# Kernel optimization log

Hardware: AMD Instinct MI355X
Metric: run time of the kernel (lower is better)

Reference implementation:

```python
import jax, jax.numpy as jnp
import numpy as np


def setup_inputs() -> dict:
    key = jax.random.key(0)
    kq, kk, kv, km = jax.random.split(key, 4)
    B, H, S, D = 2, 16, 2048, 64
    q = jax.random.normal(kq, (B, H, S, D), dtype=jnp.float32)
    k = jax.random.normal(kk, (B, H, S, D), dtype=jnp.float32)
    v = jax.random.normal(kv, (B, H, S, D), dtype=jnp.float32)
    mask = jax.random.randint(km, (B, 1, S, D * S // D), 0, 2).astype(bool)
    return {"q": q, "k": k, "v": v, "mask": mask, "d_k": 64}


def reference(q, k, v, mask, d_k):
    # score = q @ k^T / sqrt(d_k), masked_fill(mask, -1e9)
    scale = jnp.float32(1.0 / np.sqrt(d_k))
    score = jnp.einsum("bhsd,bhtd->bhst", q, k) * scale  # [B,H,S,S]
    score = jnp.where(mask, jnp.float32(-1e9), score)
    attention = jax.nn.softmax(score, axis=-1)
    # NOTE: original module (faithfully) multiplies the RAW masked score by v,
    # not the softmaxed attention: results = score @ v
    results = jnp.einsum("bhst,bhtd->bhsd", score, v)
    return (results, attention)
```

## Files before the change

kernel.cpp:

```cpp
#include <hip/hip_runtime.h>

typedef __attribute__((ext_vector_type(8))) short short8;
typedef __attribute__((ext_vector_type(4))) float f32x4;

#define S_LEN 2048
#define DH 64

__device__ __forceinline__ unsigned short f2bf(float x) {
  unsigned u = __builtin_bit_cast(unsigned, x);
  u += 0x7fffu + ((u >> 16) & 1u);
  return (unsigned short)(u >> 16);
}

__global__ void detect_stride_k(const unsigned char* __restrict__ m, int* flag) {
  __shared__ int any;
  if (threadIdx.x == 0) any = 0;
  __syncthreads();
  int acc = 0;
  for (int i = threadIdx.x; i < 4096; i += 256)
    if (i & 3) acc |= m[i];
  if (acc) atomicOr(&any, 1);
  __syncthreads();
  if (threadIdx.x == 0) *flag = any ? 1 : 4;
}

__global__ void prep_kernel(const float* __restrict__ k,
                            const float* __restrict__ v,
                            const unsigned char* __restrict__ m,
                            const int* __restrict__ flagp,
                            char* __restrict__ kbf,
                            char* __restrict__ vtbf,
                            unsigned* __restrict__ bits) {
  int bid = blockIdx.x;
  if (bid < 2048) {
    int idx = bid * 256 + threadIdx.x;
    const float4* s = (const float4*)k + (size_t)idx * 2;
    float4 a = s[0], b = s[1];
    int4 o;
    o.x = (int)f2bf(a.x) | ((int)f2bf(a.y) << 16);
    o.y = (int)f2bf(a.z) | ((int)f2bf(a.w) << 16);
    o.z = (int)f2bf(b.x) | ((int)f2bf(b.y) << 16);
    o.w = (int)f2bf(b.z) | ((int)f2bf(b.w) << 16);
    ((int4*)kbf)[idx] = o;
  } else if (bid < 6144) {
    int gt = (bid - 2048) * 256 + threadIdx.x;
    int wid = gt >> 6;
    int lane = gt & 63;
    int bh = wid >> 9;
    int rem = wid & 511;
    int d0 = (rem >> 5) * 4;
    int t = (rem & 31) * 64 + lane;
    float4 val = *(const float4*)(v + ((size_t)bh * S_LEN + t) * DH + d0);
    unsigned short* o = (unsigned short*)vtbf;
    size_t base = ((size_t)bh * DH + d0) * S_LEN + t;
    o[base]             = f2bf(val.x);
    o[base + S_LEN]     = f2bf(val.y);
    o[base + 2 * S_LEN] = f2bf(val.z);
    o[base + 3 * S_LEN] = f2bf(val.w);
  } else {
    int idx = (bid - 6144) * 256 + threadIdx.x;
    unsigned wword = 0;
    if (*flagp == 1) {
      const uint4* p = (const uint4*)(m + (size_t)idx * 32);
      uint4 a = p[0], bq = p[1];
      unsigned arr[8] = {a.x, a.y, a.z, a.w, bq.x, bq.y, bq.z, bq.w};
#pragma unroll
      for (int d = 0; d < 8; ++d)
#pragma unroll
        for (int j = 0; j < 4; ++j)
          wword |= (((arr[d] >> (8 * j)) & 255u) != 0u ? 1u : 0u) << (d * 4 + j);
    } else {
      const uint4* p = (const uint4*)m + (size_t)idx * 8;
#pragma unroll
      for (int d = 0; d < 8; ++d) {
        uint4 vv = p[d];
        wword |= (vv.x ? 1u : 0u) << (d * 4);
        wword |= (vv.y ? 1u : 0u) << (d * 4 + 1);
        wword |= (vv.z ? 1u : 0u) << (d * 4 + 2);
        wword |= (vv.w ? 1u : 0u) << (d * 4 + 3);
      }
    }
    bits[idx] = wword;
  }
}

__global__ __launch_bounds__(512, 4)
void attn_fused(const float* __restrict__ qsrc,
                const unsigned* __restrict__ mbits,
                const char* __restrict__ kbf,
                const char* __restrict__ vtbf,
                float* __restrict__ out) {
  __shared__ __align__(16) char smem[81920];

  const int tid = threadIdx.x;
  const int lane = tid & 63;
  const int w = tid >> 6;
  const int l15 = lane & 15;
  const int g = lane >> 4;
  const int sw = (l15 & 7) << 4;

  int raw = blockIdx.x;
  int swz = (raw & 7) * 64 + (raw >> 3);
  const int bh = swz >> 4;
  const int qblk = swz & 15;
  const int b = bh >> 4;
  const int q0 = qblk * 128 + w * 16;

  const char* ksrc_bh = kbf + (size_t)bh * (S_LEN * DH * 2);
  const char* vsrc_bh = vtbf + (size_t)bh * (DH * S_LEN * 2);
  char* pb = smem + 65536 + w * 2048;

  const unsigned* mrow = mbits + (size_t)b * (S_LEN * (S_LEN / 32)) +
                         (size_t)(q0 + l15) * (S_LEN / 32);

  auto stageK = [&](int buf, int t0) {
    char* dst = smem + buf * 16384;
#pragma unroll
    for (int it = 0; it < 2; ++it) {
      int o = (w * 2 + it) * 1024 + lane * 16;
      int r = o >> 7;
      int inner = o & 127;
      const char* gp = ksrc_bh + (size_t)t0 * 128 + r * 128 + (inner ^ ((r & 7) << 4));
      __builtin_amdgcn_global_load_lds((const unsigned*)gp,
                                       (unsigned*)(dst + (w * 2 + it) * 1024), 16, 0, 0);
    }
  };
  auto stageV = [&](int buf, int t0) {
    char* dst = smem + 32768 + buf * 16384;
#pragma unroll
    for (int it = 0; it < 2; ++it) {
      int o = (w * 2 + it) * 1024 + lane * 16;
      int r = o >> 8;
      int inner = o & 255;
      const char* gp = vsrc_bh + (size_t)t0 * 2 + (size_t)r * (S_LEN * 2) +
                       (inner ^ ((r & 7) << 4));
      __builtin_amdgcn_global_load_lds((const unsigned*)gp,
                                       (unsigned*)(dst + (w * 2 + it) * 1024), 16, 0, 0);
    }
  };

  short8 qf[2];
#pragma unroll
  for (int kc = 0; kc < 2; ++kc) {
    const float* qp = qsrc + ((size_t)bh * S_LEN + q0 + l15) * DH + 32 * kc + 8 * g;
    float4 x = *(const float4*)qp;
    float4 y = *(const float4*)(qp + 4);
    short8 f;
    f[0] = (short)f2bf(x.x); f[1] = (short)f2bf(x.y);
    f[2] = (short)f2bf(x.z); f[3] = (short)f2bf(x.w);
    f[4] = (short)f2bf(y.x); f[5] = (short)f2bf(y.y);
    f[6] = (short)f2bf(y.z); f[7] = (short)f2bf(y.w);
    qf[kc] = f;
  }

  f32x4 acc[4];
#pragma unroll
  for (int i = 0; i < 4; ++i) acc[i] = (f32x4){0.f, 0.f, 0.f, 0.f};
  float lp = 0.f;

  stageK(0, 0);
  stageV(0, 0);
  uint4 mw = *(const uint4*)mrow;
  __syncthreads();
  int cur = 0;

  for (int t0 = 0; t0 < S_LEN; t0 += 128) {
    uint4 mw_n;
    if (t0 + 128 < S_LEN) {
      stageK(cur ^ 1, t0 + 128);
      stageV(cur ^ 1, t0 + 128);
      mw_n = *(const uint4*)(mrow + (t0 + 128) / 32);
    }
    const char* kbuf = smem + cur * 16384;
    const char* vbuf = smem + 32768 + cur * 16384;

    f32x4 sf[8];
#pragma unroll
    for (int tc = 0; tc < 8; ++tc) {
      const char* rowp = kbuf + (16 * tc + l15) * 128;
      short8 a0 = *(const short8*)(rowp + ((16 * g) ^ sw));
      short8 a1 = *(const short8*)(rowp + ((64 + 16 * g) ^ sw));
      f32x4 z = (f32x4){0.f, 0.f, 0.f, 0.f};
      f32x4 t00 = __builtin_amdgcn_mfma_f32_16x16x32_bf16(a0, qf[0], z, 0, 0, 0);
      sf[tc] = __builtin_amdgcn_mfma_f32_16x16x32_bf16(a1, qf[1], t00, 0, 0, 0);
    }

    const unsigned mwa[4] = {mw.x, mw.y, mw.z, mw.w};
#pragma unroll
    for (int h = 0; h < 2; ++h) {
      char* pbr = pb + l15 * 128;
#pragma unroll
      for (int tq = 0; tq < 4; ++tq) {
        const int tc = 4 * h + tq;
        unsigned nib = (mwa[tc >> 1] >> (16 * (tc & 1) + 4 * g)) & 15u;
        float s0 = (nib & 1u) ? -1e9f : sf[tc][0] * 0.125f;
        float s1 = (nib & 2u) ? -1e9f : sf[tc][1] * 0.125f;
        float s2 = (nib & 4u) ? -1e9f : sf[tc][2] * 0.125f;
        float s3 = (nib & 8u) ? -1e9f : sf[tc][3] * 0.125f;
        lp += __expf(s0) + __expf(s1) + __expf(s2) + __expf(s3);
        int2 pk;
        pk.x = (int)f2bf(s0) | ((int)f2bf(s1) << 16);
        pk.y = (int)f2bf(s2) | ((int)f2bf(s3) << 16);
        *(int2*)(pbr + ((32 * tq + 8 * g) ^ sw)) = pk;
      }
      short8 p0 = *(const short8*)(pb + l15 * 128 + ((16 * g) ^ sw));
      short8 p1 = *(const short8*)(pb + l15 * 128 + ((64 + 16 * g) ^ sw));
#pragma unroll
      for (int dr = 0; dr < 4; ++dr) {
        const char* vr = vbuf + (16 * dr + l15) * 256;
        short8 v0 = *(const short8*)(vr + ((h * 128 + 16 * g) ^ sw));
        short8 v1 = *(const short8*)(vr + ((h * 128 + 64 + 16 * g) ^ sw));
        acc[dr] = __builtin_amdgcn_mfma_f32_16x16x32_bf16(v0, p0, acc[dr], 0, 0, 0);
        acc[dr] = __builtin_amdgcn_mfma_f32_16x16x32_bf16(v1, p1, acc[dr], 0, 0, 0);
      }
    }

    mw = mw_n;
    __syncthreads();
    cur ^= 1;
  }

  float l = lp;
  l += __shfl_xor(l, 16);
  l += __shfl_xor(l, 32);
  const float inv = 1.0f / l;

#pragma unroll
  for (int dr = 0; dr < 4; ++dr) {
    float4 o;
    o.x = acc[dr][0]; o.y = acc[dr][1];
    o.z = acc[dr][2]; o.w = acc[dr][3];
    *(float4*)(out + ((size_t)bh * S_LEN + q0 + l15) * DH + 16 * dr + 4 * g) = o;
  }

  float* att = out + (size_t)4194304 + (size_t)bh * S_LEN * S_LEN;

  float invr[4];
#pragma unroll
  for (int r = 0; r < 4; ++r) invr[r] = __shfl(inv, 4 * g + r, 64);

  const unsigned* mrowB = mbits + (size_t)b * (S_LEN * (S_LEN / 32)) +
                          (size_t)(q0 + 4 * g) * (S_LEN / 32);

  stageK(0, 0);
  __syncthreads();
  cur = 0;

  for (int t0 = 0; t0 < S_LEN; t0 += 128) {
    if (t0 + 128 < S_LEN) stageK(cur ^ 1, t0 + 128);
    const char* kbuf = smem + cur * 16384;

    uint4 mv[4];
#pragma unroll
    for (int r = 0; r < 4; ++r) mv[r] = *(const uint4*)(mrowB + r * 64 + t0 / 32);

    float* attT = att + (size_t)(q0 + 4 * g) * S_LEN + t0 + l15;

#pragma unroll
    for (int tc = 0; tc < 8; ++tc) {
      const char* rowp = kbuf + (16 * tc + l15) * 128;
      short8 b0 = *(const short8*)(rowp + ((16 * g) ^ sw));
      short8 b1 = *(const short8*)(rowp + ((64 + 16 * g) ^ sw));
      f32x4 z = (f32x4){0.f, 0.f, 0.f, 0.f};
      f32x4 t0f = __builtin_amdgcn_mfma_f32_16x16x32_bf16(qf[0], b0, z, 0, 0, 0);
      f32x4 sff = __builtin_amdgcn_mfma_f32_16x16x32_bf16(qf[1], b1, t0f, 0, 0, 0);
      const int bitsh = 16 * (tc & 1) + l15;
#pragma unroll
      for (int r = 0; r < 4; ++r) {
        unsigned word = (tc >> 1) == 0 ? mv[r].x : (tc >> 1) == 1 ? mv[r].y
                      : (tc >> 1) == 2 ? mv[r].z : mv[r].w;
        float s = ((word >> bitsh) & 1u) ? -1e9f : sff[r] * 0.125f;
        attT[(size_t)r * S_LEN + 16 * tc] = __expf(s) * invr[r];
      }
    }

    __syncthreads();
    cur ^= 1;
  }
}

extern "C" void kernel_launch(void* const* d_in, const int* in_sizes, int n_in,
                              void* d_out, int out_size, void* d_ws, size_t ws_size,
                              hipStream_t stream) {
  (void)in_sizes; (void)n_in; (void)out_size; (void)ws_size;
  const float* q = (const float*)d_in[0];
  const float* k = (const float*)d_in[1];
  const float* v = (const float*)d_in[2];
  const unsigned char* mask = (const unsigned char*)d_in[3];
  float* out = (float*)d_out;

  char* ws = (char*)d_ws;
  int* flag = (int*)ws;
  char* kbf = ws + 256;
  char* vtbf = ws + 256 + 8 * 1024 * 1024;
  unsigned* bits = (unsigned*)(ws + 256 + 16 * 1024 * 1024);

  detect_stride_k<<<1, 256, 0, stream>>>(mask, flag);
  prep_kernel<<<7168, 256, 0, stream>>>(k, v, mask, flag, kbf, vtbf, bits);
  attn_fused<<<512, 512, 0, stream>>>(q, bits, kbf, vtbf, out);
}
```

Before: 206.7 us.

## Split key tile across wave pairs, each wave handling 32 query rows

Each pair of waves now shares 32 query rows and divides every 128-key tile into two 64-key halves, so each wave computes two 16-row query sub-tiles. Every K/V fragment read from LDS therefore feeds twice as many MFMAs. The two halves' partial PV accumulators and row sums are combined through shared memory after the main loop. The mask words for the attention pass are also prefetched one tile ahead. This costs more registers for the doubled accumulators, plus extra LDS traffic and a barrier for the reduction.

Result: slower. 270.0 us (+30.7%).

```diff
diff --git a/kernel.cpp b/kernel.cpp
--- a/kernel.cpp
+++ b/kernel.cpp
@@ -95,6 +95,8 @@
   const int tid = threadIdx.x;
   const int lane = tid & 63;
   const int w = tid >> 6;
+  const int qw = w >> 1;
+  const int tw = w & 1;
   const int l15 = lane & 15;
   const int g = lane >> 4;
   const int sw = (l15 & 7) << 4;
@@ -104,14 +106,17 @@
   const int bh = swz >> 4;
   const int qblk = swz & 15;
   const int b = bh >> 4;
-  const int q0 = qblk * 128 + w * 16;
+  const int q0 = qblk * 128 + qw * 32;
 
   const char* ksrc_bh = kbf + (size_t)bh * (S_LEN * DH * 2);
   const char* vsrc_bh = vtbf + (size_t)bh * (DH * S_LEN * 2);
   char* pb = smem + 65536 + w * 2048;
-
-  const unsigned* mrow = mbits + (size_t)b * (S_LEN * (S_LEN / 32)) +
-                         (size_t)(q0 + l15) * (S_LEN / 32);
+  float* sums = (float*)(smem + 65536);
+  float* invl = (float*)(smem + 66048);
+
+  const unsigned* mb_b = mbits + (size_t)b * (S_LEN * (S_LEN / 32));
+  const unsigned* mrow0 = mb_b + (size_t)(q0 + l15) * 64;
+  const unsigned* mrow1 = mb_b + (size_t)(q0 + 16 + l15) * 64;
 
   auto stageK = [&](int buf, int t0) {
     char* dst = smem + buf * 16384;
@@ -139,141 +144,199 @@
     }
   };
 
-  short8 qf[2];
-#pragma unroll
-  for (int kc = 0; kc < 2; ++kc) {
-    const float* qp = qsrc + ((size_t)bh * S_LEN + q0 + l15) * DH + 32 * kc + 8 * g;
-    float4 x = *(const float4*)qp;
-    float4 y = *(const float4*)(qp + 4);
-    short8 f;
-    f[0] = (short)f2bf(x.x); f[1] = (short)f2bf(x.y);
-    f[2] = (short)f2bf(x.z); f[3] = (short)f2bf(x.w);
-    f[4] = (short)f2bf(y.x); f[5] = (short)f2bf(y.y);
-    f[6] = (short)f2bf(y.z); f[7] = (short)f2bf(y.w);
-    qf[kc] = f;
-  }
-
-  f32x4 acc[4];
-#pragma unroll
-  for (int i = 0; i < 4; ++i) acc[i] = (f32x4){0.f, 0.f, 0.f, 0.f};
-  float lp = 0.f;
+  short8 qf[2][2];
+#pragma unroll
+  for (int qs = 0; qs < 2; ++qs)
+#pragma unroll
+    for (int kc = 0; kc < 2; ++kc) {
+      const float* qp = qsrc + ((size_t)bh * S_LEN + q0 + 16 * qs + l15) * DH + 32 * kc + 8 * g;
+      float4 x = *(const float4*)qp;
+      float4 y = *(const float4*)(qp + 4);
+      short8 f;
+      f[0] = (short)f2bf(x.x); f[1] = (short)f2bf(x.y);
+      f[2] = (short)f2bf(x.z); f[3] = (short)f2bf(x.w);
+      f[4] = (short)f2bf(y.x); f[5] = (short)f2bf(y.y);
+      f[6] = (short)f2bf(y.z); f[7] = (short)f2bf(y.w);
+      qf[qs][kc] = f;
+    }
+
+  f32x4 acc[4][2];
+#pragma unroll
+  for (int i = 0; i < 4; ++i)
+#pragma unroll
+    for (int j = 0; j < 2; ++j) acc[i][j] = (f32x4){0.f, 0.f, 0.f, 0.f};
+  float lp0 = 0.f, lp1 = 0.f;
 
   stageK(0, 0);
   stageV(0, 0);
-  uint4 mw = *(const uint4*)mrow;
+  uint2 mw0 = *(const uint2*)(mrow0 + 2 * tw);
+  uint2 mw1 = *(const uint2*)(mrow1 + 2 * tw);
   __syncthreads();
   int cur = 0;
 
   for (int t0 = 0; t0 < S_LEN; t0 += 128) {
-    uint4 mw_n;
+    uint2 mwn0, mwn1;
     if (t0 + 128 < S_LEN) {
       stageK(cur ^ 1, t0 + 128);
       stageV(cur ^ 1, t0 + 128);
-      mw_n = *(const uint4*)(mrow + (t0 + 128) / 32);
+      mwn0 = *(const uint2*)(mrow0 + (t0 + 128) / 32 + 2 * tw);
+      mwn1 = *(const uint2*)(mrow1 + (t0 + 128) / 32 + 2 * tw);
     }
     const char* kbuf = smem + cur * 16384;
     const char* vbuf = smem + 32768 + cur * 16384;
 
-    f32x4 sf[8];
-#pragma unroll
-    for (int tc = 0; tc < 8; ++tc) {
-      const char* rowp = kbuf + (16 * tc + l15) * 128;
+    f32x4 sf[2][4];
+#pragma unroll
+    for (int tc = 0; tc < 4; ++tc) {
+      const char* rowp = kbuf + (64 * tw + 16 * tc + l15) * 128;
       short8 a0 = *(const short8*)(rowp + ((16 * g) ^ sw));
       short8 a1 = *(const short8*)(rowp + ((64 + 16 * g) ^ sw));
       f32x4 z = (f32x4){0.f, 0.f, 0.f, 0.f};
-      f32x4 t00 = __builtin_amdgcn_mfma_f32_16x16x32_bf16(a0, qf[0], z, 0, 0, 0);
-      sf[tc] = __builtin_amdgcn_mfma_f32_16x16x32_bf16(a1, qf[1], t00, 0, 0, 0);
-    }
-
-    const unsigned mwa[4] = {mw.x, mw.y, mw.z, mw.w};
-#pragma unroll
-    for (int h = 0; h < 2; ++h) {
-      char* pbr = pb + l15 * 128;
-#pragma unroll
-      for (int tq = 0; tq < 4; ++tq) {
-        const int tc = 4 * h + tq;
-        unsigned nib = (mwa[tc >> 1] >> (16 * (tc & 1) + 4 * g)) & 15u;
-        float s0 = (nib & 1u) ? -1e9f : sf[tc][0] * 0.125f;
-        float s1 = (nib & 2u) ? -1e9f : sf[tc][1] * 0.125f;
-        float s2 = (nib & 4u) ? -1e9f : sf[tc][2] * 0.125f;
-        float s3 = (nib & 8u) ? -1e9f : sf[tc][3] * 0.125f;
-        lp += __expf(s0) + __expf(s1) + __expf(s2) + __expf(s3);
+      f32x4 t00 = __builtin_amdgcn_mfma_f32_16x16x32_bf16(a0, qf[0][0], z, 0, 0, 0);
+      sf[0][tc] = __builtin_amdgcn_mfma_f32_16x16x32_bf16(a1, qf[0][1], t00, 0, 0, 0);
+      f32x4 t10 = __builtin_amdgcn_mfma_f32_16x16x32_bf16(a0, qf[1][0], z, 0, 0, 0);
+      sf[1][tc] = __builtin_amdgcn_mfma_f32_16x16x32_bf16(a1, qf[1][1], t10, 0, 0, 0);
+    }
+
+    char* pbr = pb + l15 * 128;
+    short8 p0[2], p1[2];
+#pragma unroll
+    for (int qs = 0; qs < 2; ++qs) {
+      const uint2 mwq = qs ? mw1 : mw0;
+#pragma unroll
+      for (int tc = 0; tc < 4; ++tc) {
+        unsigned word = (tc < 2) ? mwq.x : mwq.y;
+        unsigned nib = (word >> (16 * (tc & 1) + 4 * g)) & 15u;
+        float s0 = (nib & 1u) ? -1e9f : sf[qs][tc][0] * 0.125f;
+        float s1 = (nib & 2u) ? -1e9f : sf[qs][tc][1] * 0.125f;
+        float s2 = (nib & 4u) ? -1e9f : sf[qs][tc][2] * 0.125f;
+        float s3 = (nib & 8u) ? -1e9f : sf[qs][tc][3] * 0.125f;
+        float e = __expf(s0) + __expf(s1) + __expf(s2) + __expf(s3);
+        if (qs) lp1 += e; else lp0 += e;
         int2 pk;
         pk.x = (int)f2bf(s0) | ((int)f2bf(s1) << 16);
         pk.y = (int)f2bf(s2) | ((int)f2bf(s3) << 16);
-        *(int2*)(pbr + ((32 * tq + 8 * g) ^ sw)) = pk;
+        *(int2*)(pbr + ((32 * tc + 8 * g) ^ sw)) = pk;
       }
-      short8 p0 = *(const short8*)(pb + l15 * 128 + ((16 * g) ^ sw));
-      short8 p1 = *(const short8*)(pb + l15 * 128 + ((64 + 16 * g) ^ sw));
-#pragma unroll
-      for (int dr = 0; dr < 4; ++dr) {
-        const char* vr = vbuf + (16 * dr + l15) * 256;
-        short8 v0 = *(const short8*)(vr + ((h * 128 + 16 * g) ^ sw));
-        short8 v1 = *(const short8*)(vr + ((h * 128 + 64 + 16 * g) ^ sw));
-        acc[dr] = __builtin_amdgcn_mfma_f32_16x16x32_bf16(v0, p0, acc[dr], 0, 0, 0);
-        acc[dr] = __builtin_amdgcn_mfma_f32_16x16x32_bf16(v1, p1, acc[dr], 0, 0, 0);
-      }
-    }
-
-    mw = mw_n;
+      p0[qs] = *(const short8*)(pb + l15 * 128 + ((16 * g) ^ sw));
+      p1[qs] = *(const short8*)(pb + l15 * 128 + ((64 + 16 * g) ^ sw));
+    }
+
+#pragma unroll
+    for (int dr = 0; dr < 4; ++dr) {
+      const char* vr = vbuf + (16 * dr + l15) * 256 + 128 * tw;
+      short8 v0 = *(const short8*)(vr + ((16 * g) ^ sw));
+      short8 v1 = *(const short8*)(vr + ((64 + 16 * g) ^ sw));
+      acc[dr][0] = __builtin_amdgcn_mfma_f32_16x16x32_bf16(
+          v1, p1[0], __builtin_amdgcn_mfma_f32_16x16x32_bf16(v0, p0[0], acc[dr][0], 0, 0, 0), 0, 0, 0);
+      acc[dr][1] = __builtin_amdgcn_mfma_f32_16x16x32_bf16(
+          v1, p1[1], __builtin_amdgcn_mfma_f32_16x16x32_bf16(v0, p0[1], acc[dr][1], 0, 0, 0), 0, 0, 0);
+    }
+
+    mw0 = mwn0; mw1 = mwn1;
     __syncthreads();
     cur ^= 1;
   }
 
-  float l = lp;
-  l += __shfl_xor(l, 16);
-  l += __shfl_xor(l, 32);
-  const float inv = 1.0f / l;
-
-#pragma unroll
-  for (int dr = 0; dr < 4; ++dr) {
-    float4 o;
-    o.x = acc[dr][0]; o.y = acc[dr][1];
-    o.z = acc[dr][2]; o.w = acc[dr][3];
-    *(float4*)(out + ((size_t)bh * S_LEN + q0 + l15) * DH + 16 * dr + 4 * g) = o;
-  }
+  lp0 += __shfl_xor(lp0, 16); lp0 += __shfl_xor(lp0, 32);
+  lp1 += __shfl_xor(lp1, 16); lp1 += __shfl_xor(lp1, 32);
+
+  if (tw == 1) {
+    if (lane < 16) {
+      sums[qw * 32 + l15] = lp0;
+      sums[qw * 32 + 16 + l15] = lp1;
+    }
+    char* ar = smem + 32768 + qw * 8192;
+#pragma unroll
+    for (int dr = 0; dr < 4; ++dr)
+#pragma unroll
+      for (int qs = 0; qs < 2; ++qs)
+        *(f32x4*)(ar + (16 * qs + l15) * 256 + (((16 * dr + 4 * g) * 4) ^ ((l15 & 7) << 4))) = acc[dr][qs];
+  }
+  __syncthreads();
+  if (tw == 0) {
+    const char* ar = smem + 32768 + qw * 8192;
+#pragma unroll
+    for (int dr = 0; dr < 4; ++dr)
+#pragma unroll
+      for (int qs = 0; qs < 2; ++qs)
+        acc[dr][qs] += *(const f32x4*)(ar + (16 * qs + l15) * 256 + (((16 * dr + 4 * g) * 4) ^ ((l15 & 7) << 4)));
+    float tot0 = lp0 + sums[qw * 32 + l15];
+    float tot1 = lp1 + sums[qw * 32 + 16 + l15];
+    float i0 = 1.0f / tot0;
+    float i1 = 1.0f / tot1;
+    if (lane < 16) {
+      invl[qw * 32 + l15] = i0;
+      invl[qw * 32 + 16 + l15] = i1;
+    }
+#pragma unroll
+    for (int dr = 0; dr < 4; ++dr) {
+      float4 o0, o1;
+      o0.x = acc[dr][0][0]; o0.y = acc[dr][0][1]; o0.z = acc[dr][0][2]; o0.w = acc[dr][0][3];
+      o1.x = acc[dr][1][0]; o1.y = acc[dr][1][1]; o1.z = acc[dr][1][2]; o1.w = acc[dr][1][3];
+      *(float4*)(out + ((size_t)bh * S_LEN + q0 + l15) * DH + 16 * dr + 4 * g) = o0;
+      *(float4*)(out + ((size_t)bh * S_LEN + q0 + 16 + l15) * DH + 16 * dr + 4 * g) = o1;
+    }
+  }
+  __syncthreads();
 
   float* att = out + (size_t)4194304 + (size_t)bh * S_LEN * S_LEN;
-
-  float invr[4];
-#pragma unroll
-  for (int r = 0; r < 4; ++r) invr[r] = __shfl(inv, 4 * g + r, 64);
-
-  const unsigned* mrowB = mbits + (size_t)b * (S_LEN * (S_LEN / 32)) +
-                          (size_t)(q0 + 4 * g) * (S_LEN / 32);
+  float invq0[4], invq1[4];
+#pragma unroll
+  for (int r = 0; r < 4; ++r) {
+    invq0[r] = invl[qw * 32 + 4 * g + r];
+    invq1[r] = invl[qw * 32 + 16 + 4 * g + r];
+  }
+  float* attq0 = att + (size_t)(q0 + 4 * g) * S_LEN + l15;
+  float* attq1 = att + (size_t)(q0 + 16 + 4 * g) * S_LEN + l15;
 
   stageK(0, 0);
+  uint2 mv0[4], mv1[4];
+#pragma unroll
+  for (int r = 0; r < 4; ++r) {
+    mv0[r] = *(const uint2*)(mb_b + (size_t)(q0 + 4 * g + r) * 64 + 2 * tw);
+    mv1[r] = *(const uint2*)(mb_b + (size_t)(q0 + 16 + 4 * g + r) * 64 + 2 * tw);
+  }
   __syncthreads();
   cur = 0;
 
   for (int t0 = 0; t0 < S_LEN; t0 += 128) {
-    if (t0 + 128 < S_LEN) stageK(cur ^ 1, t0 + 128);
+    uint2 nv0[4], nv1[4];
+    if (t0 + 128 < S_LEN) {
+      stageK(cur ^ 1, t0 + 128);
+#pragma unroll
+      for (int r = 0; r < 4; ++r) {
+        nv0[r] = *(const uint2*)(mb_b + (size_t)(q0 + 4 * g + r) * 64 + (t0 + 128) / 32 + 2 * tw);
+        nv1[r] = *(const uint2*)(mb_b + (size_t)(q0 + 16 + 4 * g + r) * 64 + (t0 + 128) / 32 + 2 * tw);
+      }
+    }
     const char* kbuf = smem + cur * 16384;
 
-    uint4 mv[4];
-#pragma unroll
-    for (int r = 0; r < 4; ++r) mv[r] = *(const uint4*)(mrowB + r * 64 + t0 / 32);
-
-    float* attT = att + (size_t)(q0 + 4 * g) * S_LEN + t0 + l15;
-
-#pragma unroll
-    for (int tc = 0; tc < 8; ++tc) {
-      const char* rowp = kbuf + (16 * tc + l15) * 128;
+#pragma unroll
+    for (int tc = 0; tc < 4; ++tc) {
+      const char* rowp = kbuf + (64 * tw + 16 * tc + l15) * 128;
       short8 b0 = *(const short8*)(rowp + ((16 * g) ^ sw));
       short8 b1 = *(const short8*)(rowp + ((64 + 16 * g) ^ sw));
       f32x4 z = (f32x4){0.f, 0.f, 0.f, 0.f};
-      f32x4 t0f = __builtin_amdgcn_mfma_f32_16x16x32_bf16(qf[0], b0, z, 0, 0, 0);
-      f32x4 sff = __builtin_amdgcn_mfma_f32_16x16x32_bf16(qf[1], b1, t0f, 0, 0, 0);
-      const int bitsh = 16 * (tc & 1) + l15;
+      f32x4 t0f = __builtin_amdgcn_mfma_f32_16x16x32_bf16(qf[0][0], b0, z, 0, 0, 0);
+      f32x4 s0f = __builtin_amdgcn_mfma_f32_16x16x32_bf16(qf[0][1], b1, t0f, 0, 0, 0);
+      f32x4 t1f = __builtin_amdgcn_mfma_f32_16x16x32_bf16(qf[1][0], b0, z, 0, 0, 0);
+      f32x4 s1f = __builtin_amdgcn_mfma_f32_16x16x32_bf16(qf[1][1], b1, t1f, 0, 0, 0);
+      const int off = t0 + 64 * tw + 16 * tc;
+      const int sh = 16 * (tc & 1) + l15;
 #pragma unroll
       for (int r = 0; r < 4; ++r) {
-        unsigned word = (tc >> 1) == 0 ? mv[r].x : (tc >> 1) == 1 ? mv[r].y
-                      : (tc >> 1) == 2 ? mv[r].z : mv[r].w;
-        float s = ((word >> bitsh) & 1u) ? -1e9f : sff[r] * 0.125f;
-        attT[(size_t)r * S_LEN + 16 * tc] = __expf(s) * invr[r];
+        unsigned w0 = (tc < 2) ? mv0[r].x : mv0[r].y;
+        float sa = ((w0 >> sh) & 1u) ? -1e9f : s0f[r] * 0.125f;
+        attq0[(size_t)r * S_LEN + off] = __expf(sa) * invq0[r];
+        unsigned w1 = (tc < 2) ? mv1[r].x : mv1[r].y;
+        float sb = ((w1 >> sh) & 1u) ? -1e9f : s1f[r] * 0.125f;
+        attq1[(size_t)r * S_LEN + off] = __expf(sb) * invq1[r];
       }
     }
 
+#pragma unroll
+    for (int r = 0; r < 4; ++r) { mv0[r] = nv0[r]; mv1[r] = nv1[r]; }
     __syncthreads();
     cur ^= 1;
   }
```
